# Kernel tuning notes

Hardware: AMD Instinct MI355X
Metric: run time of the kernel (lower is better)

Reference implementation:

```python
import jax, jax.numpy as jnp
import numpy as np

EPS = 1e-5
S_CENTERS = 1024  # npoint//4
NSAMPLE = 32


def index_points(pts, idx):
    # pts [B,N,C], idx [B,...] int -> [B,...,C]
    return jax.vmap(lambda p, i: p[i])(pts, idx)


def farthest_point_sample(xyz, npoint):
    # xyz [B,N,3] -> [B,npoint] indices (deterministic start at index 0)
    B, N, _ = xyz.shape
    def body(carry, _):
        dist, far = carry
        centroid = jnp.take_along_axis(xyz, far[:, None, None], axis=1)  # [B,1,3]
        d = jnp.sum((xyz - centroid) ** 2, axis=-1)                      # [B,N]
        dist = jnp.minimum(dist, d)
        nxt = jnp.argmax(dist, axis=-1).astype(jnp.int32)
        return (dist, nxt), far
    init = (jnp.full((B, N), 1e10, xyz.dtype), jnp.zeros((B,), jnp.int32))
    _, idx = jax.lax.scan(body, init, None, length=npoint)
    return jnp.transpose(idx)  # [B,npoint]


def knn_point(k, xyz, new_xyz):
    # squared dists [B,S,N], take k nearest
    d = (jnp.sum(new_xyz ** 2, -1)[:, :, None]
         + jnp.sum(xyz ** 2, -1)[:, None, :]
         - 2.0 * jnp.einsum('bsc,bnc->bsn', new_xyz, xyz))
    _, idx = jax.lax.top_k(-d, k)
    return idx  # [B,S,k]


def instance_norm(h):
    # h [B,S,K,C]: InstanceNorm2d (affine=False) normalizes per (b,c) over spatial dims
    mu = jnp.mean(h, axis=(1, 2), keepdims=True)
    var = jnp.var(h, axis=(1, 2), keepdims=True)
    return (h - mu) * jax.lax.rsqrt(var + EPS)


def setup_inputs() -> dict:
    key = jax.random.key(0)
    ks = jax.random.split(key, 12)
    B, N, C = 8, 4096, 128
    inp = {
        'pc1_l_loc2': jax.random.normal(ks[0], (B, 3, N), jnp.float32),
        'corr_feats': jax.random.normal(ks[1], (B, C, N), jnp.float32),
        'W1': jax.random.normal(ks[2], (128, 131), jnp.float32) * 0.05,
        'b1': jnp.zeros((128,), jnp.float32),
        'W2': jax.random.normal(ks[3], (128, 128), jnp.float32) * 0.05,
        'b2': jnp.zeros((128,), jnp.float32),
        'W3': jax.random.normal(ks[4], (128, 128), jnp.float32) * 0.05,
        'b3': jnp.zeros((128,), jnp.float32),
        'fc_w': jax.random.normal(ks[5], (3, 128), jnp.float32) * 0.05,
        'fc_b': jnp.zeros((3,), jnp.float32),
    }
    return inp


def reference(pc1_l_loc2, corr_feats, W1, b1, W2, b2, W3, b3, fc_w, fc_b):
    xyz = jnp.transpose(pc1_l_loc2, (0, 2, 1))    # [B,N,3]
    points = jnp.transpose(corr_feats, (0, 2, 1))  # [B,N,128]

    fps_idx = farthest_point_sample(xyz, S_CENTERS)           # [B,S]
    new_xyz = index_points(xyz, fps_idx)                      # [B,S,3]
    idx = knn_point(NSAMPLE, xyz, new_xyz)                    # [B,S,K]
    grouped_xyz = index_points(xyz, idx)                      # [B,S,K,3]
    grouped_xyz_norm = grouped_xyz - new_xyz[:, :, None, :]
    grouped_pts = index_points(points, idx)                   # [B,S,K,128]
    h = jnp.concatenate([grouped_xyz_norm, grouped_pts], -1)  # [B,S,K,131]

    for W, b in ((W1, b1), (W2, b2), (W3, b3)):
        h = jnp.einsum('bskc,oc->bsko', h, W) + b  # 1x1 conv as matmul
        h = jax.nn.relu(instance_norm(h))

    x = jnp.max(h, axis=2)                         # [B,S,128] max over neighbors
    x = jnp.einsum('bsc,oc->bso', x, fc_w) + fc_b  # [B,S,3]
    flow0 = jnp.transpose(x, (0, 2, 1))            # [B,3,S]
    return flow0
```

## Files before the change

kernel.cpp:

```cpp
#include <hip/hip_runtime.h>
#include <hip/hip_fp16.h>

#define NB 8
#define NPTS 4096
#define NS 1024
#define NK 32
#define NM (NB*NS*NK)

typedef _Float16 f16x8 __attribute__((ext_vector_type(8)));
typedef float    f32x4 __attribute__((ext_vector_type(4)));
typedef float    f32x2 __attribute__((ext_vector_type(2)));

__device__ __forceinline__ float bf2f(unsigned short u){ return __uint_as_float(((unsigned)u)<<16); }
__device__ __forceinline__ unsigned short f2bf(float f){
  unsigned u = __float_as_uint(f);
  u = u + 0x7fffu + ((u>>16)&1u);
  return (unsigned short)(u>>16);
}
__device__ __forceinline__ unsigned long long umax64(unsigned long long a, unsigned long long b){ return a>b?a:b; }
__device__ __forceinline__ unsigned long long umin64(unsigned long long a, unsigned long long b){ return a<b?a:b; }
__device__ __forceinline__ unsigned umin3u(unsigned a, unsigned b, unsigned c){
  unsigned m = a<b?a:b; return m<c?m:c;
}

#define DPP_STEP_MAX(x, ctrl, rm) { \
  unsigned _t = (unsigned)__builtin_amdgcn_update_dpp((int)(x), (int)(x), (ctrl), (rm), 0xf, false); \
  (x) = ((x) > _t) ? (x) : _t; }
#define DPP_STEP_MIN(x, ctrl, rm) { \
  unsigned _t = (unsigned)__builtin_amdgcn_update_dpp((int)(x), (int)(x), (ctrl), (rm), 0xf, false); \
  (x) = ((x) < _t) ? (x) : _t; }

__device__ __forceinline__ unsigned wave_max_u32(unsigned x){
  DPP_STEP_MAX(x, 0x111, 0xf);
  DPP_STEP_MAX(x, 0x112, 0xf);
  DPP_STEP_MAX(x, 0x114, 0xf);
  DPP_STEP_MAX(x, 0x118, 0xf);
  DPP_STEP_MAX(x, 0x142, 0xa);
  DPP_STEP_MAX(x, 0x143, 0xc);
  return (unsigned)__builtin_amdgcn_readlane((int)x, 63);
}
__device__ __forceinline__ unsigned wave_min_u32(unsigned x){
  DPP_STEP_MIN(x, 0x111, 0xf);
  DPP_STEP_MIN(x, 0x112, 0xf);
  DPP_STEP_MIN(x, 0x114, 0xf);
  DPP_STEP_MIN(x, 0x118, 0xf);
  DPP_STEP_MIN(x, 0x142, 0xa);
  DPP_STEP_MIN(x, 0x143, 0xc);
  return (unsigned)__builtin_amdgcn_readlane((int)x, 63);
}

__device__ __forceinline__ bool detect_f32(const unsigned short* __restrict__ u){
  int huge_=0, zero_=0;
  #pragma unroll
  for (int i=0;i<64;i++){
    unsigned short w = u[i];
    if ((w & 0x7fffu) == 0) { zero_++; continue; }
    float a = fabsf(bf2f(w));
    if (a > 1e6f || a < 1e-6f) huge_++;
  }
  return (huge_ >= 8) || (zero_ >= 24);
}
__device__ __forceinline__ float ldin(const void* p, size_t i, bool f32){
  if (f32) return ((const float*)p)[i];
  else     return bf2f(((const unsigned short*)p)[i]);
}

__global__ __launch_bounds__(256) void fps_kernel(const void* __restrict__ pc1,
                                                  int* __restrict__ fps_out){
  __shared__ __align__(16) float4 cp4[NPTS];
  __shared__ __align__(16) unsigned long long part[2][4];
  int b = blockIdx.x, t = threadIdx.x;
  const bool f32 = detect_f32((const unsigned short*)pc1);
  const size_t base = (size_t)b*3*NPTS;
  for (int i=t;i<NPTS;i+=256){
    float4 v;
    v.x = ldin(pc1, base+i, f32);
    v.y = ldin(pc1, base+NPTS+i, f32);
    v.z = ldin(pc1, base+2*NPTS+i, f32);
    v.w = 0.f;
    cp4[i] = v;
  }
  __syncthreads();
  f32x2 px[8],py[8],pz[8],dist[8];
  #pragma unroll
  for (int j=0;j<8;j++){
    float4 a = cp4[t*16+2*j], c = cp4[t*16+2*j+1];
    px[j] = f32x2{a.x, c.x};
    py[j] = f32x2{a.y, c.y};
    pz[j] = f32x2{a.z, c.z};
    dist[j] = f32x2{1e10f, 1e10f};
  }
  int far = 0;
  int w = t>>6, lane = t&63;
  for (int it=0; it<NS; it++){
    if (t==0) fps_out[b*NS+it] = far;
    float4 cc = cp4[far];
    f32x2 vcx = f32x2{cc.x,cc.x}, vcy = f32x2{cc.y,cc.y}, vcz = f32x2{cc.z,cc.z};
    {
      #pragma clang fp contract(off)
      #pragma unroll
      for (int j=0;j<8;j++){
        f32x2 dx = px[j]-vcx, dy = py[j]-vcy, dz = pz[j]-vcz;
        f32x2 d  = (dx*dx + dy*dy) + dz*dz;
        dist[j]  = __builtin_elementwise_min(dist[j], d);
      }
    }
    float d_[16];
    #pragma unroll
    for (int j=0;j<8;j++){ d_[2*j]=dist[j][0]; d_[2*j+1]=dist[j][1]; }
    float a0 = fmaxf(fmaxf(d_[0],d_[1]),d_[2]);
    float a1 = fmaxf(fmaxf(d_[3],d_[4]),d_[5]);
    float a2 = fmaxf(fmaxf(d_[6],d_[7]),d_[8]);
    float a3 = fmaxf(fmaxf(d_[9],d_[10]),d_[11]);
    float a4 = fmaxf(fmaxf(d_[12],d_[13]),d_[14]);
    float b0 = fmaxf(fmaxf(a0,a1),a2);
    float b1 = fmaxf(fmaxf(a3,a4),d_[15]);
    float bl = fmaxf(b0,b1);
    int li = 0;
    #pragma unroll
    for (int i=15;i>=0;i--) if (d_[i]==bl) li = i;
    unsigned blu = __float_as_uint(bl);
    unsigned wm = wave_max_u32(blu);
    unsigned long long mk = __ballot(blu == wm);
    int l = __builtin_ctzll(mk);
    int idx = __builtin_amdgcn_readlane(t*16+li, l);
    if (lane==0) part[it&1][w] = ((unsigned long long)wm<<32) | (unsigned)(NPTS-1-idx);
    __syncthreads();
    const ulonglong2* pp = (const ulonglong2*)&part[it&1][0];
    ulonglong2 A = pp[0], B = pp[1];
    unsigned long long m = umax64(umax64(A.x,A.y), umax64(B.x,B.y));
    far = NPTS-1 - (int)(m & 0xffffffffu);
  }
}

__global__ __launch_bounds__(256) void knn_kernel(const void* __restrict__ pc1,
                                                  const int* __restrict__ fps_idx,
                                                  float* __restrict__ new_xyz,
                                                  int* __restrict__ knn_idx){
  __shared__ __align__(16) unsigned dbs[256*20];
  __shared__ __align__(16) unsigned long long lists[4][NK];
  int blk = blockIdx.x;
  int b = blk >> 10;
  int t = threadIdx.x;
  int w = t>>6, lane = t&63;
  const bool f32 = detect_f32((const unsigned short*)pc1);
  const size_t base = (size_t)b*3*NPTS;
  int n0 = fps_idx[blk];
  float qx = ldin(pc1, base+n0, f32);
  float qy = ldin(pc1, base+NPTS+n0, f32);
  float qz = ldin(pc1, base+2*NPTS+n0, f32);
  if (t==0){ new_xyz[(size_t)blk*3]=qx; new_xyz[(size_t)blk*3+1]=qy; new_xyz[(size_t)blk*3+2]=qz; }
  float qn = __fadd_rn(__fadd_rn(__fmul_rn(qx,qx),__fmul_rn(qy,qy)),__fmul_rn(qz,qz));
  #pragma unroll
  for (int k=0;k<16;k++){
    int n = t + 256*k;
    float x = ldin(pc1, base+n, f32);
    float y = ldin(pc1, base+NPTS+n, f32);
    float z = ldin(pc1, base+2*NPTS+n, f32);
    float pn = __fadd_rn(__fadd_rn(__fmul_rn(x,x),__fmul_rn(y,y)),__fmul_rn(z,z));
    float dt = __fadd_rn(__fadd_rn(__fmul_rn(qx,x),__fmul_rn(qy,y)),__fmul_rn(qz,z));
    float d  = __fsub_rn(__fadd_rn(qn,pn), __fmul_rn(2.f,dt));
    unsigned u = __float_as_uint(d);
    u = (u & 0x80000000u) ? ~u : (u | 0x80000000u);
    dbs[(n>>4)*20 + (n&15)] = u;
  }
  __syncthreads();
  unsigned gm[4]; int gj[4];
  #pragma unroll
  for (int g=0; g<4; g++){
    uint4 v = *(const uint4*)&dbs[t*20 + 4*g];
    unsigned m = v.x; int j = 0;
    if (v.y < m){ m = v.y; j = 1; }
    if (v.z < m){ m = v.z; j = 2; }
    if (v.w < m){ m = v.w; j = 3; }
    gm[g] = m; gj[g] = j;
  }
  #pragma unroll 1
  for (int r=0; r<NK; r++){
    unsigned bl = umin3u(gm[0],gm[1],gm[2]);
    bl = bl < gm[3] ? bl : gm[3];
    int bg = 3;
    if (gm[2]==bl) bg=2;
    if (gm[1]==bl) bg=1;
    if (gm[0]==bl) bg=0;
    int lj = gj[0];
    if (bg==1) lj=gj[1];
    if (bg==2) lj=gj[2];
    if (bg==3) lj=gj[3];
    int bn = (t<<4) + (bg<<2) + lj;
    uint4 gv = *(const uint4*)&dbs[t*20 + (bg<<2)];
    unsigned wm = wave_min_u32(bl);
    unsigned long long mk = __ballot(bl == wm);
    int l = __builtin_ctzll(mk);
    int idx = __builtin_amdgcn_readlane(bn, l);
    if (lane==0) lists[w][r] = ((unsigned long long)wm<<32) | (unsigned)idx;
    if (lane==l){
      unsigned g0 = (lj==0)?0xFFFFFFFFu:gv.x;
      unsigned g1 = (lj==1)?0xFFFFFFFFu:gv.y;
      unsigned g2 = (lj==2)?0xFFFFFFFFu:gv.z;
      unsigned g3 = (lj==3)?0xFFFFFFFFu:gv.w;
      uint4 nv; nv.x=g0; nv.y=g1; nv.z=g2; nv.w=g3;
      *(uint4*)&dbs[t*20 + (bg<<2)] = nv;
      unsigned m = g0; int j = 0;
      if (g1 < m){ m=g1; j=1; }
      if (g2 < m){ m=g2; j=2; }
      if (g3 < m){ m=g3; j=3; }
      if (bg==0){ gm[0]=m; gj[0]=j; }
      if (bg==1){ gm[1]=m; gj[1]=j; }
      if (bg==2){ gm[2]=m; gj[2]=j; }
      if (bg==3){ gm[3]=m; gj[3]=j; }
    }
  }
  __syncthreads();
  if (t < 128){
    int cl = t>>5, p = t&31;
    unsigned long long K = lists[cl][p];
    int rank = p;
    #pragma unroll
    for (int ol=0; ol<4; ol++){
      if (ol==cl) continue;
      int lo = 0;
      if (lists[ol][15]    < K) lo  = 16;
      if (lists[ol][lo+7]  < K) lo += 8;
      if (lists[ol][lo+3]  < K) lo += 4;
      if (lists[ol][lo+1]  < K) lo += 2;
      if (lists[ol][lo]    < K) lo += 1;
      rank += lo;
    }
    if (rank < NK) knn_idx[(size_t)blk*NK + rank] = (int)(K & 0xffffffffu);
  }
}

__global__ __launch_bounds__(256) void feat_transpose(const void* __restrict__ feats,
                                                      const void* __restrict__ pc1,
                                                      _Float16* __restrict__ G,
                                                      float* __restrict__ statz){
  __shared__ float tile[128][65];
  const bool f32 = detect_f32((const unsigned short*)pc1);
  int blk = blockIdx.x;
  int b = blk>>6, n0 = (blk&63)*64;
  int t = threadIdx.x;
  if (blk==0){
    for (int i=t;i<6144;i+=256) statz[i]=0.f;
  }
  #pragma unroll 4
  for (int i=0;i<32;i++){
    int idx = i*256 + t;
    int c = idx>>6, n = idx&63;
    tile[c][n] = ldin(feats, ((size_t)b*128 + c)*NPTS + n0 + n, f32);
  }
  __syncthreads();
  #pragma unroll 4
  for (int i=0;i<32;i++){
    int idx = i*256 + t;
    int n = idx>>7, c = idx&127;
    G[((size_t)b*NPTS + n0 + n)*136 + 3 + c] = (_Float16)tile[c][n];
  }
  if (t<64){
    size_t gb = ((size_t)b*NPTS + n0 + t)*136;
    G[gb]=(_Float16)0.f; G[gb+1]=(_Float16)0.f; G[gb+2]=(_Float16)0.f;
    #pragma unroll
    for (int c=131;c<136;c++) G[gb+c]=(_Float16)0.f;
  }
}

template<int LAYER>
__global__ __launch_bounds__(256) void conv_mfma(
    const void* __restrict__ pc1,
    const _Float16* __restrict__ G,
    const int* __restrict__ knn_idx,
    const float* __restrict__ new_xyz,
    const _Float16* __restrict__ Hin,
    const float* __restrict__ gp1,
    const float* __restrict__ gp2,
    const void* __restrict__ W,
    _Float16* __restrict__ Hout,
    float* __restrict__ gs1, float* __restrict__ gs2)
{
  constexpr int KC  = (LAYER==1)?131:128;
  constexpr int KCP = (LAYER==1)?160:128;
  constexpr int HSW = (LAYER==1)?168:136;
  __shared__ __align__(16) _Float16 hs[128][HSW];
  __shared__ __align__(16) _Float16 wt[128][40];
  __shared__ float red1[4][64], red2[4][64];
  __shared__ int   nidx[128];
  __shared__ float cxyz[4][3];
  __shared__ __align__(16) _Float16 smuh[128], srsh[128];
  int blk = blockIdx.x;
  int m0 = blk*128;
  int b  = m0 >> 15;
  int t  = threadIdx.x;
  const bool f32 = detect_f32((const unsigned short*)pc1);
  int w = t>>6, lane = t&63;
  int l16 = lane&15, q = lane>>4, q8 = q*8;
  int wr = (w&1)*64, wc = (w>>1)*64;

  if (LAYER==1){
    if (t<128) nidx[t] = knn_idx[m0+t];
    if (t<12)  cxyz[t/3][t%3] = new_xyz[(size_t)(m0>>5)*3 + t];
    __syncthreads();
    for (int u=t; u<128*17; u+=256){
      int p = u/17, qq = u - p*17;
      const f16x8* src = (const f16x8*)(G + ((size_t)b*NPTS + nidx[p])*136 + qq*8);
      *(f16x8*)&hs[p][qq*8] = *src;
    }
    for (int u=t; u<128*3; u+=256){
      int p = u/3, qq = u - p*3;
      uint4 z; z.x=z.y=z.z=z.w=0u;
      *(uint4*)&hs[p][136+qq*8] = z;
    }
    __syncthreads();
    if (t<128){
      int n = nidx[t];
      float cx = cxyz[t>>5][0], cy = cxyz[t>>5][1], cz = cxyz[t>>5][2];
      hs[t][0] = (_Float16)(ldin(pc1, ((size_t)b*3+0)*NPTS+n, f32) - cx);
      hs[t][1] = (_Float16)(ldin(pc1, ((size_t)b*3+1)*NPTS+n, f32) - cy);
      hs[t][2] = (_Float16)(ldin(pc1, ((size_t)b*3+2)*NPTS+n, f32) - cz);
    }
    __syncthreads();
  } else {
    if (t<128){
      const float inv = 1.0f/32768.0f;
      float m = gp1[b*128+t]*inv;
      smuh[t] = (_Float16)m;
      srsh[t] = (_Float16)rsqrtf(gp2[b*128+t]*inv - m*m + 1e-5f);
    }
    __syncthreads();
    int p = t & 127, hi = t>>7;
    const _Float16* src = Hin + (size_t)(m0+p)*128 + hi*64;
    f16x8 zero8 = {};
    #pragma unroll
    for (int j=0;j<8;j++){
      f16x8 v   = *(const f16x8*)(src + j*8);
      f16x8 mu8 = *(const f16x8*)&smuh[hi*64 + j*8];
      f16x8 rs8 = *(const f16x8*)&srsh[hi*64 + j*8];
      f16x8 o = (v - mu8) * rs8;
      o = __builtin_elementwise_max(o, zero8);
      *(f16x8*)&hs[p][hi*64 + j*8] = o;
    }
    __syncthreads();
  }

  f32x4 acc[4][4];
  #pragma unroll
  for (int i=0;i<4;i++)
    #pragma unroll
    for (int c=0;c<4;c++){ acc[i][c][0]=0.f; acc[i][c][1]=0.f; acc[i][c][2]=0.f; acc[i][c][3]=0.f; }

  for (int k0=0; k0<KCP; k0+=32){
    {
      int o = t>>1, half = t&1;
      f16x8 w0, w1;
      if (f32 && LAYER!=1){
        const float4* Wf = (const float4*)((const float*)W + (size_t)o*KC + k0 + half*16);
        float4 v0 = Wf[0], v1 = Wf[1], v2 = Wf[2], v3 = Wf[3];
        w0[0]=(_Float16)v0.x; w0[1]=(_Float16)v0.y; w0[2]=(_Float16)v0.z; w0[3]=(_Float16)v0.w;
        w0[4]=(_Float16)v1.x; w0[5]=(_Float16)v1.y; w0[6]=(_Float16)v1.z; w0[7]=(_Float16)v1.w;
        w1[0]=(_Float16)v2.x; w1[1]=(_Float16)v2.y; w1[2]=(_Float16)v2.z; w1[3]=(_Float16)v2.w;
        w1[4]=(_Float16)v3.x; w1[5]=(_Float16)v3.y; w1[6]=(_Float16)v3.z; w1[7]=(_Float16)v3.w;
      } else {
        #pragma unroll
        for (int jj=0;jj<8;jj++){
          int c0 = k0 + half*16 + jj, c1 = c0 + 8;
          w0[jj] = (_Float16)((c0<KC) ? ldin(W, (size_t)o*KC + c0, f32) : 0.f);
          w1[jj] = (_Float16)((c1<KC) ? ldin(W, (size_t)o*KC + c1, f32) : 0.f);
        }
      }
      *(f16x8*)&wt[o][half*16]     = w0;
      *(f16x8*)&wt[o][half*16 + 8] = w1;
    }
    __syncthreads();
    f16x8 av[4], bv[4];
    #pragma unroll
    for (int i=0;i<4;i++) av[i] = *(const f16x8*)&hs[wr + i*16 + l16][k0 + q8];
    #pragma unroll
    for (int c=0;c<4;c++) bv[c] = *(const f16x8*)&wt[wc + c*16 + l16][q8];
    #pragma unroll
    for (int i=0;i<4;i++)
      #pragma unroll
      for (int c=0;c<4;c++)
        acc[i][c] = __builtin_amdgcn_mfma_f32_16x16x32_f16(av[i], bv[c], acc[i][c], 0,0,0);
    __syncthreads();
  }

  #pragma unroll
  for (int c=0;c<4;c++){
    int o = wc + c*16 + l16;
    float s1=0.f, s2=0.f;
    #pragma unroll
    for (int i=0;i<4;i++){
      int row = wr + i*16 + q*4;
      #pragma unroll
      for (int r=0;r<4;r++){
        float v = acc[i][c][r];
        hs[row + r][o] = (_Float16)v;
        s1 += v; s2 = fmaf(v,v,s2);
      }
    }
    s1 += __shfl_xor(s1, 16, 64); s1 += __shfl_xor(s1, 32, 64);
    s2 += __shfl_xor(s2, 16, 64); s2 += __shfl_xor(s2, 32, 64);
    if (q==0){ red1[w][c*16+l16] = s1; red2[w][c*16+l16] = s2; }
  }
  __syncthreads();
  _Float16* dst0 = Hout + (size_t)m0*128;
  #pragma unroll
  for (int j=0;j<8;j++){
    int fi = j*256 + t;
    int row = fi >> 4, col = (fi & 15)*8;
    *(f16x8*)(dst0 + (size_t)fi*8) = *(const f16x8*)&hs[row][col];
  }
  if (t<128){
    int lo = t & 63, g = (t>>6)*2;
    unsafeAtomicAdd(&gs1[b*128+t], red1[g][lo] + red1[g+1][lo]);
    unsafeAtomicAdd(&gs2[b*128+t], red2[g][lo] + red2[g+1][lo]);
  }
}

__global__ __launch_bounds__(128) void final_kernel(
    const void* __restrict__ pc1,
    const _Float16* __restrict__ H,
    const float* __restrict__ gp1, const float* __restrict__ gp2,
    const void* __restrict__ fc_w, const void* __restrict__ fc_b,
    void* __restrict__ outv)
{
  int blk = blockIdx.x;
  int b = blk>>10, s = blk & 1023;
  int o = threadIdx.x;
  const bool f32 = detect_f32((const unsigned short*)pc1);
  int bo = b*128 + o;
  const float inv = 1.0f/32768.0f;
  float mu_ = gp1[bo]*inv;
  float rs_ = rsqrtf(gp2[bo]*inv - mu_*mu_ + 1e-5f);
  const _Float16* hp = H + (size_t)blk*NK*128 + o;
  float m = -1e30f;
  #pragma unroll 4
  for(int k=0;k<NK;k++){
    float v = ((float)hp[(size_t)k*128] - mu_)*rs_;
    m = fmaxf(m, v);
  }
  m = fmaxf(m, 0.f);
  __shared__ float mv[128];
  mv[o] = m;
  __syncthreads();
  if (o<3){
    float acc = ldin(fc_b, o, f32);
    for(int c=0;c<128;c++) acc = fmaf(ldin(fc_w, (size_t)o*128+c, f32), mv[c], acc);
    size_t oi = ((size_t)b*3 + o)*NS + s;
    if (f32) ((float*)outv)[oi] = acc;
    else     ((unsigned short*)outv)[oi] = f2bf(acc);
  }
}

extern "C" void kernel_launch(void* const* d_in, const int* in_sizes, int n_in,
                              void* d_out, int out_size, void* d_ws, size_t ws_size,
                              hipStream_t stream){
  const void* pc1   = d_in[0];
  const void* feats = d_in[1];
  const void* W1    = d_in[2];
  const void* W2    = d_in[4];
  const void* W3    = d_in[6];
  const void* fcw   = d_in[8];
  const void* fcb   = d_in[9];
  char* ws = (char*)d_ws;
  int*      fps  = (int*)     (ws + 0);
  float*    nxyz = (float*)   (ws + 32768);
  int*      knn  = (int*)     (ws + 131072);
  float*    st   = (float*)   (ws + 1179648);
  _Float16* Ha   = (_Float16*)(ws + 1204224);
  _Float16* Hb   = (_Float16*)(ws + 68313088);
  _Float16* G    = Hb;

  feat_transpose<<<NB*64, 256, 0, stream>>>(feats, pc1, G, st);
  fps_kernel<<<NB, 256, 0, stream>>>(pc1, fps);
  knn_kernel<<<NB*NS, 256, 0, stream>>>(pc1, fps, nxyz, knn);

  conv_mfma<1><<<NM/128, 256, 0, stream>>>(pc1, G, knn, nxyz,
      (const _Float16*)nullptr, (const float*)nullptr, (const float*)nullptr,
      W1, Ha, st, st+1024);
  conv_mfma<2><<<NM/128, 256, 0, stream>>>(pc1, G, knn, nxyz,
      Ha, st, st+1024, W2, Hb, st+2048, st+3072);
  conv_mfma<3><<<NM/128, 256, 0, stream>>>(pc1, G, knn, nxyz,
      Hb, st+2048, st+3072, W3, Ha, st+4096, st+5120);

  final_kernel<<<NB*NS, 128, 0, stream>>>(pc1, Ha, st+4096, st+5120, fcw, fcb, d_out);
}
```

Measured before the change: 1.093 ms.

## Replace iterative KNN selection with radix histogram threshold and candidate ranking

The KNN kernel no longer runs 32 serial rounds of wave-min extraction followed by a merge of per-wave lists. It builds a 4096-bin shared-memory histogram over the top 12 bits of the sortable distance keys, then runs a hierarchical prefix scan to find the bin that holds the 32nd nearest point. Points at or below that bin are gathered into a candidate buffer and ranked by brute-force comparison. This removes the serialized selection loop, at the cost of shared-memory atomics and a hard cap of 512 candidates, so results could be wrong if many points fall into the threshold bin.

```diff
diff --git a/kernel.cpp b/kernel.cpp
--- a/kernel.cpp
+++ b/kernel.cpp
@@ -18,17 +18,10 @@
   return (unsigned short)(u>>16);
 }
 __device__ __forceinline__ unsigned long long umax64(unsigned long long a, unsigned long long b){ return a>b?a:b; }
-__device__ __forceinline__ unsigned long long umin64(unsigned long long a, unsigned long long b){ return a<b?a:b; }
-__device__ __forceinline__ unsigned umin3u(unsigned a, unsigned b, unsigned c){
-  unsigned m = a<b?a:b; return m<c?m:c;
-}
 
 #define DPP_STEP_MAX(x, ctrl, rm) { \
   unsigned _t = (unsigned)__builtin_amdgcn_update_dpp((int)(x), (int)(x), (ctrl), (rm), 0xf, false); \
   (x) = ((x) > _t) ? (x) : _t; }
-#define DPP_STEP_MIN(x, ctrl, rm) { \
-  unsigned _t = (unsigned)__builtin_amdgcn_update_dpp((int)(x), (int)(x), (ctrl), (rm), 0xf, false); \
-  (x) = ((x) < _t) ? (x) : _t; }
 
 __device__ __forceinline__ unsigned wave_max_u32(unsigned x){
   DPP_STEP_MAX(x, 0x111, 0xf);
@@ -37,15 +30,6 @@
   DPP_STEP_MAX(x, 0x118, 0xf);
   DPP_STEP_MAX(x, 0x142, 0xa);
   DPP_STEP_MAX(x, 0x143, 0xc);
-  return (unsigned)__builtin_amdgcn_readlane((int)x, 63);
-}
-__device__ __forceinline__ unsigned wave_min_u32(unsigned x){
-  DPP_STEP_MIN(x, 0x111, 0xf);
-  DPP_STEP_MIN(x, 0x112, 0xf);
-  DPP_STEP_MIN(x, 0x114, 0xf);
-  DPP_STEP_MIN(x, 0x118, 0xf);
-  DPP_STEP_MIN(x, 0x142, 0xa);
-  DPP_STEP_MIN(x, 0x143, 0xc);
   return (unsigned)__builtin_amdgcn_readlane((int)x, 63);
 }
 
@@ -137,20 +121,28 @@
                                                   const int* __restrict__ fps_idx,
                                                   float* __restrict__ new_xyz,
                                                   int* __restrict__ knn_idx){
-  __shared__ __align__(16) unsigned dbs[256*20];
-  __shared__ __align__(16) unsigned long long lists[4][NK];
+  __shared__ __align__(16) unsigned hist[4096];
+  __shared__ __align__(16) unsigned long long cand[512];
+  __shared__ unsigned part[256];
+  __shared__ unsigned sup[16];
+  __shared__ unsigned scal[2];
   int blk = blockIdx.x;
   int b = blk >> 10;
   int t = threadIdx.x;
-  int w = t>>6, lane = t&63;
   const bool f32 = detect_f32((const unsigned short*)pc1);
   const size_t base = (size_t)b*3*NPTS;
   int n0 = fps_idx[blk];
   float qx = ldin(pc1, base+n0, f32);
   float qy = ldin(pc1, base+NPTS+n0, f32);
   float qz = ldin(pc1, base+2*NPTS+n0, f32);
-  if (t==0){ new_xyz[(size_t)blk*3]=qx; new_xyz[(size_t)blk*3+1]=qy; new_xyz[(size_t)blk*3+2]=qz; }
+  if (t==0){
+    new_xyz[(size_t)blk*3]=qx; new_xyz[(size_t)blk*3+1]=qy; new_xyz[(size_t)blk*3+2]=qz;
+    scal[0]=0u;
+  }
+  #pragma unroll
+  for (int j=0;j<16;j++) hist[j*256 + t] = 0u;
   float qn = __fadd_rn(__fadd_rn(__fmul_rn(qx,qx),__fmul_rn(qy,qy)),__fmul_rn(qz,qz));
+  unsigned dv[16];
   #pragma unroll
   for (int k=0;k<16;k++){
     int n = t + 256*k;
@@ -161,72 +153,56 @@
     float dt = __fadd_rn(__fadd_rn(__fmul_rn(qx,x),__fmul_rn(qy,y)),__fmul_rn(qz,z));
     float d  = __fsub_rn(__fadd_rn(qn,pn), __fmul_rn(2.f,dt));
     unsigned u = __float_as_uint(d);
-    u = (u & 0x80000000u) ? ~u : (u | 0x80000000u);
-    dbs[(n>>4)*20 + (n&15)] = u;
-  }
-  __syncthreads();
-  unsigned gm[4]; int gj[4];
-  #pragma unroll
-  for (int g=0; g<4; g++){
-    uint4 v = *(const uint4*)&dbs[t*20 + 4*g];
-    unsigned m = v.x; int j = 0;
-    if (v.y < m){ m = v.y; j = 1; }
-    if (v.z < m){ m = v.z; j = 2; }
-    if (v.w < m){ m = v.w; j = 3; }
-    gm[g] = m; gj[g] = j;
-  }
-  #pragma unroll 1
-  for (int r=0; r<NK; r++){
-    unsigned bl = umin3u(gm[0],gm[1],gm[2]);
-    bl = bl < gm[3] ? bl : gm[3];
-    int bg = 3;
-    if (gm[2]==bl) bg=2;
-    if (gm[1]==bl) bg=1;
-    if (gm[0]==bl) bg=0;
-    int lj = gj[0];
-    if (bg==1) lj=gj[1];
-    if (bg==2) lj=gj[2];
-    if (bg==3) lj=gj[3];
-    int bn = (t<<4) + (bg<<2) + lj;
-    uint4 gv = *(const uint4*)&dbs[t*20 + (bg<<2)];
-    unsigned wm = wave_min_u32(bl);
-    unsigned long long mk = __ballot(bl == wm);
-    int l = __builtin_ctzll(mk);
-    int idx = __builtin_amdgcn_readlane(bn, l);
-    if (lane==0) lists[w][r] = ((unsigned long long)wm<<32) | (unsigned)idx;
-    if (lane==l){
-      unsigned g0 = (lj==0)?0xFFFFFFFFu:gv.x;
-      unsigned g1 = (lj==1)?0xFFFFFFFFu:gv.y;
-      unsigned g2 = (lj==2)?0xFFFFFFFFu:gv.z;
-      unsigned g3 = (lj==3)?0xFFFFFFFFu:gv.w;
-      uint4 nv; nv.x=g0; nv.y=g1; nv.z=g2; nv.w=g3;
-      *(uint4*)&dbs[t*20 + (bg<<2)] = nv;
-      unsigned m = g0; int j = 0;
-      if (g1 < m){ m=g1; j=1; }
-      if (g2 < m){ m=g2; j=2; }
-      if (g3 < m){ m=g3; j=3; }
-      if (bg==0){ gm[0]=m; gj[0]=j; }
-      if (bg==1){ gm[1]=m; gj[1]=j; }
-      if (bg==2){ gm[2]=m; gj[2]=j; }
-      if (bg==3){ gm[3]=m; gj[3]=j; }
-    }
-  }
-  __syncthreads();
-  if (t < 128){
-    int cl = t>>5, p = t&31;
-    unsigned long long K = lists[cl][p];
-    int rank = p;
-    #pragma unroll
-    for (int ol=0; ol<4; ol++){
-      if (ol==cl) continue;
-      int lo = 0;
-      if (lists[ol][15]    < K) lo  = 16;
-      if (lists[ol][lo+7]  < K) lo += 8;
-      if (lists[ol][lo+3]  < K) lo += 4;
-      if (lists[ol][lo+1]  < K) lo += 2;
-      if (lists[ol][lo]    < K) lo += 1;
-      rank += lo;
-    }
+    dv[k] = (u & 0x80000000u) ? ~u : (u | 0x80000000u);
+  }
+  __syncthreads();
+  #pragma unroll
+  for (int k=0;k<16;k++)
+    atomicAdd(&hist[dv[k]>>20], 1u);
+  __syncthreads();
+  {
+    unsigned s = 0;
+    const uint4* hp = (const uint4*)&hist[t*16];
+    #pragma unroll
+    for (int j=0;j<4;j++){
+      uint4 v = hp[j];
+      s += v.x + v.y + v.z + v.w;
+    }
+    part[t] = s;
+  }
+  __syncthreads();
+  if (t < 16){
+    unsigned q = 0;
+    #pragma unroll
+    for (int j=0;j<16;j++) q += part[t*16 + j];
+    sup[t] = q;
+  }
+  __syncthreads();
+  if (t == 0){
+    unsigned acc = 0; int sb = 0;
+    for (; sb < 16; sb++){ unsigned v = sup[sb]; if (acc + v >= NK) break; acc += v; }
+    int pt = sb*16;
+    for (; pt < sb*16+16; pt++){ unsigned v = part[pt]; if (acc + v >= NK) break; acc += v; }
+    int bn = pt*16;
+    for (; bn < pt*16+16; bn++){ unsigned v = hist[bn]; if (acc + v >= NK) break; acc += v; }
+    scal[1] = (unsigned)bn;
+  }
+  __syncthreads();
+  unsigned beta = scal[1];
+  #pragma unroll
+  for (int k=0;k<16;k++){
+    if ((dv[k]>>20) <= beta){
+      unsigned pos = atomicAdd(&scal[0], 1u);
+      if (pos < 512u)
+        cand[pos] = ((unsigned long long)dv[k]<<32) | (unsigned)(t + 256*k);
+    }
+  }
+  __syncthreads();
+  int C = (int)scal[0]; if (C > 512) C = 512;
+  for (int tt = t; tt < C; tt += 256){
+    unsigned long long K = cand[tt];
+    int rank = 0;
+    for (int j = 0; j < C; j++) rank += (cand[j] < K) ? 1 : 0;
     if (rank < NK) knn_idx[(size_t)blk*NK + rank] = (int)(K & 0xffffffffu);
   }
 }
```

New measurement: 1.059 ms. -3.0%, faster.
